# Performance work log

Measured on AMD Instinct MI355X. Metric: run time of the kernel, lower is better.

Reference implementation:

```python
import jax, jax.numpy as jnp
import numpy as np

N_HEADS = 12

def setup_inputs() -> dict:
    key = jax.random.key(0)
    ks = jax.random.split(key, 5)
    B, T, H = 8, 1024, 768
    x = jax.random.normal(ks[0], (B, T, H), dtype=jnp.float32)
    # PyTorch Linear init: U(-1/sqrt(fan_in), 1/sqrt(fan_in))
    s1 = 1.0 / np.sqrt(H)
    W_attn = jax.random.uniform(ks[1], (H, 3 * H), minval=-s1, maxval=s1, dtype=jnp.float32)
    b_attn = jax.random.uniform(ks[2], (3 * H,), minval=-s1, maxval=s1, dtype=jnp.float32)
    W_proj = jax.random.uniform(ks[3], (H, H), minval=-s1, maxval=s1, dtype=jnp.float32)
    b_proj = jax.random.uniform(ks[4], (H,), minval=-s1, maxval=s1, dtype=jnp.float32)
    return {"x": x, "W_attn": W_attn, "b_attn": b_attn, "W_proj": W_proj, "b_proj": b_proj}

def reference(x, W_attn, b_attn, W_proj, b_proj):
    B, T, H = x.shape
    nh = N_HEADS
    Hs = H // nh
    qkv = x @ W_attn + b_attn                       # [B,T,3H]
    q, k, v = jnp.split(qkv, 3, axis=-1)            # each [B,T,H]
    # -> [B, nh, T, Hs]
    q = q.reshape(B, T, nh, Hs).transpose(0, 2, 1, 3)
    k = k.reshape(B, T, nh, Hs).transpose(0, 2, 1, 3)
    v = v.reshape(B, T, nh, Hs).transpose(0, 2, 1, 3)
    scale = 1.0 / jnp.sqrt(jnp.asarray(Hs, dtype=x.dtype))
    scores = jnp.einsum("bhqd,bhkd->bhqk", q, k) * scale  # [B,nh,T,T]
    causal = jnp.tril(jnp.ones((T, T), dtype=bool))
    scores = jnp.where(causal, scores, jnp.asarray(-jnp.inf, dtype=scores.dtype))
    attn = jax.nn.softmax(scores, axis=-1)
    out = jnp.einsum("bhqk,bhkd->bhqd", attn, v)    # [B,nh,T,Hs]
    out = out.transpose(0, 2, 1, 3).reshape(B, T, H)
    return out @ W_proj + b_proj
```

## Files before the change

kernel.cpp:

```cpp
#include <hip/hip_runtime.h>
#include <math.h>


typedef __attribute__((ext_vector_type(4))) float  f32x4;
typedef __attribute__((ext_vector_type(8))) short  bf16x8;
typedef __attribute__((ext_vector_type(4))) short  bf16x4;
typedef __attribute__((ext_vector_type(4))) unsigned int u32x4;

__device__ __forceinline__ unsigned short f2bf(float f) {
    union { float f; unsigned u; } v; v.f = f;
    unsigned r = (v.u + 0x7FFFu + ((v.u >> 16) & 1u)) >> 16;
    return (unsigned short)r;
}

__device__ __forceinline__ void glds16(const unsigned short* g, unsigned short* l) {
    __builtin_amdgcn_global_load_lds((const __attribute__((address_space(1))) void*)g,
                                     (__attribute__((address_space(3))) void*)l, 16, 0, 0);
}

__global__ __launch_bounds__(256)
void cvt_f32_bf16(const float* __restrict__ in, unsigned short* __restrict__ out) {
    const int i = blockIdx.x * 256 + threadIdx.x;
    const float4 v = ((const float4*)in)[i];
    ushort4 o;
    o.x = f2bf(v.x); o.y = f2bf(v.y); o.z = f2bf(v.z); o.w = f2bf(v.w);
    ((ushort4*)out)[i] = o;
}

__global__ __launch_bounds__(256)
void transpose_w(const float* __restrict__ W, unsigned short* __restrict__ Wt,
                 int K, int N) {
    __shared__ float Ts[64][65];
    const int k0 = blockIdx.x * 64, n0 = blockIdx.y * 64;
    const int t = threadIdx.x;
    const int r = t >> 4, cg = (t & 15) * 4;
#pragma unroll
    for (int p = 0; p < 4; ++p) {
        const float4 v = *(const float4*)(&W[(size_t)(k0 + r + p * 16) * N + n0 + cg]);
        Ts[r + p * 16][cg + 0] = v.x;
        Ts[r + p * 16][cg + 1] = v.y;
        Ts[r + p * 16][cg + 2] = v.z;
        Ts[r + p * 16][cg + 3] = v.w;
    }
    __syncthreads();
#pragma unroll
    for (int p = 0; p < 4; ++p) {
        const int n = n0 + r + p * 16;
        ushort4 o;
        o.x = f2bf(Ts[cg + 0][r + p * 16]);
        o.y = f2bf(Ts[cg + 1][r + p * 16]);
        o.z = f2bf(Ts[cg + 2][r + p * 16]);
        o.w = f2bf(Ts[cg + 3][r + p * 16]);
        *(ushort4*)(&Wt[(size_t)n * K + k0 + cg]) = o;
    }
}

__global__ __launch_bounds__(256)
void gemm_bf16(const unsigned short* __restrict__ A, const unsigned short* __restrict__ Bt,
               const float* __restrict__ bias, void* __restrict__ Cout,
               int M, int N, int K, int out_bf16) {
    __shared__ unsigned short As[128 * 32];
    __shared__ unsigned short Bs[128 * 32];

    const int t = threadIdx.x;
    const int L = t & 63, w = t >> 6;
    const int l15 = L & 15, quad = L >> 4;
    const int wy = w & 1, wx = w >> 1;
    const int m0 = blockIdx.x * 128, n0 = blockIdx.y * 128;

    const int srow = t >> 2, koff = (t & 3) * 8;
    const unsigned short* ag = A + (size_t)(m0 + srow) * K + koff;
    const unsigned short* bg = Bt + (size_t)(n0 + srow) * K + koff;
    unsigned short* as0 = As + srow * 32 + koff;
    unsigned short* bs0 = Bs + srow * 32 + koff;
    const size_t gstep = (size_t)64 * K;

    f32x4 acc[4][4];
#pragma unroll
    for (int mt = 0; mt < 4; ++mt)
#pragma unroll
        for (int nt = 0; nt < 4; ++nt) acc[mt][nt] = (f32x4){0.f, 0.f, 0.f, 0.f};

    for (int k0 = 0; k0 < K; k0 += 32) {
        glds16(ag + k0,         as0);
        glds16(ag + gstep + k0, as0 + 64 * 32);
        glds16(bg + k0,         bs0);
        glds16(bg + gstep + k0, bs0 + 64 * 32);
        __syncthreads();

        bf16x8 af[4], bfr[4];
#pragma unroll
        for (int mt = 0; mt < 4; ++mt)
            af[mt] = *(const bf16x8*)(As + (wy * 64 + mt * 16 + l15) * 32 + quad * 8);
#pragma unroll
        for (int nt = 0; nt < 4; ++nt)
            bfr[nt] = *(const bf16x8*)(Bs + (wx * 64 + nt * 16 + l15) * 32 + quad * 8);
#pragma unroll
        for (int mt = 0; mt < 4; ++mt)
#pragma unroll
            for (int nt = 0; nt < 4; ++nt)
                acc[mt][nt] = __builtin_amdgcn_mfma_f32_16x16x32_bf16(af[mt], bfr[nt], acc[mt][nt], 0, 0, 0);
        __syncthreads();
    }

    float bv[4];
#pragma unroll
    for (int nt = 0; nt < 4; ++nt) bv[nt] = bias[n0 + wx * 64 + nt * 16 + l15];
#pragma unroll
    for (int mt = 0; mt < 4; ++mt) {
        const int mrow = m0 + wy * 64 + mt * 16 + quad * 4;
#pragma unroll
        for (int r = 0; r < 4; ++r) {
            const int m = mrow + r;
            if (out_bf16) {
                unsigned short* C = (unsigned short*)Cout;
#pragma unroll
                for (int nt = 0; nt < 4; ++nt)
                    C[(size_t)m * N + n0 + wx * 64 + nt * 16 + l15] = f2bf(acc[mt][nt][r] + bv[nt]);
            } else {
                float* C = (float*)Cout;
#pragma unroll
                for (int nt = 0; nt < 4; ++nt)
                    C[(size_t)m * N + n0 + wx * 64 + nt * 16 + l15] = acc[mt][nt][r] + bv[nt];
            }
        }
    }
}

__global__ __launch_bounds__(256)
void attn_mfma(const unsigned short* __restrict__ qkv, unsigned short* __restrict__ attb) {
    const int T = 1024, QKVW = 2304, NH = 12, H = 768;
    __shared__ unsigned short Ks[64 * 64];
    __shared__ unsigned short Vt[64 * 72];

    const int t = threadIdx.x;
    const int L = t & 63, w = t >> 6;
    const int l15 = L & 15, quad = L >> 4;
    const int pair = blockIdx.x & 7;
    const int bh = blockIdx.x >> 3;
    const int h = bh % NH, b = bh / NH;

    const unsigned short* base = qkv + (size_t)b * T * QKVW + h * 64;

    const int g0 = t,        r0 = g0 >> 3, lc0 = (g0 & 7) ^ (r0 & 7);
    const int g1 = 256 + t,  r1 = g1 >> 3, lc1 = (g1 & 7) ^ (r1 & 7);
    const float SM = 0.18033688f;

    for (int sub = 0; sub < 2; ++sub) {
        const int qt = sub ? pair : 15 - pair;
        const int q0 = qt * 64;

        __syncthreads();
        glds16(base + (size_t)(q0 + r0) * QKVW + lc0 * 8, Ks + g0 * 8);
        glds16(base + (size_t)(q0 + r1) * QKVW + lc1 * 8, Ks + g1 * 8);
        __syncthreads();

        bf16x8 qf[2];
        {
            const int qrow = 16 * w + l15;
            qf[0] = *(const bf16x8*)(Ks + qrow * 64 + ((quad    ) ^ (qrow & 7)) * 8);
            qf[1] = *(const bf16x8*)(Ks + qrow * 64 + ((quad + 4) ^ (qrow & 7)) * 8);
        }

        f32x4 ot[4];
#pragma unroll
        for (int dt = 0; dt < 4; ++dt) ot[dt] = (f32x4){0.f, 0.f, 0.f, 0.f};
        float mrun = -1e30f, lsum = 0.f;

        for (int j0 = 0; j0 <= q0; j0 += 64) {
            __syncthreads();
            glds16(base + (size_t)(j0 + r0) * QKVW + 768 + lc0 * 8, Ks + g0 * 8);
            glds16(base + (size_t)(j0 + r1) * QKVW + 768 + lc1 * 8, Ks + g1 * 8);
            {
                const int k4 = (t & 15) * 4, d4 = (t >> 4) * 4;
                const unsigned short* vb = base + 1536 + d4;
                const ushort4 a0 = *(const ushort4*)(vb + (size_t)(j0 + k4 + 0) * QKVW);
                const ushort4 a1 = *(const ushort4*)(vb + (size_t)(j0 + k4 + 1) * QKVW);
                const ushort4 a2 = *(const ushort4*)(vb + (size_t)(j0 + k4 + 2) * QKVW);
                const ushort4 a3 = *(const ushort4*)(vb + (size_t)(j0 + k4 + 3) * QKVW);
                ushort4 c0, c1, c2, c3;
                c0.x = a0.x; c0.y = a1.x; c0.z = a2.x; c0.w = a3.x;
                c1.x = a0.y; c1.y = a1.y; c1.z = a2.y; c1.w = a3.y;
                c2.x = a0.z; c2.y = a1.z; c2.z = a2.z; c2.w = a3.z;
                c3.x = a0.w; c3.y = a1.w; c3.z = a2.w; c3.w = a3.w;
                *(ushort4*)(Vt + (size_t)(d4 + 0) * 72 + k4) = c0;
                *(ushort4*)(Vt + (size_t)(d4 + 1) * 72 + k4) = c1;
                *(ushort4*)(Vt + (size_t)(d4 + 2) * 72 + k4) = c2;
                *(ushort4*)(Vt + (size_t)(d4 + 3) * 72 + k4) = c3;
            }
            __syncthreads();

            f32x4 st[4];
#pragma unroll
            for (int mt = 0; mt < 4; ++mt) {
                st[mt] = (f32x4){0.f, 0.f, 0.f, 0.f};
                const int krow = 16 * mt + l15;
                const bf16x8 kf0 = *(const bf16x8*)(Ks + krow * 64 + ((quad    ) ^ (krow & 7)) * 8);
                const bf16x8 kf1 = *(const bf16x8*)(Ks + krow * 64 + ((quad + 4) ^ (krow & 7)) * 8);
                st[mt] = __builtin_amdgcn_mfma_f32_16x16x32_bf16(kf0, qf[0], st[mt], 0, 0, 0);
                st[mt] = __builtin_amdgcn_mfma_f32_16x16x32_bf16(kf1, qf[1], st[mt], 0, 0, 0);
            }

            if (j0 == q0) {
                const int qin = 16 * w + l15;
#pragma unroll
                for (int mt = 0; mt < 4; ++mt)
#pragma unroll
                    for (int r = 0; r < 4; ++r)
                        if (16 * mt + 4 * quad + r > qin) st[mt][r] = -1e30f;
            }

            float nm = st[0][0];
#pragma unroll
            for (int mt = 0; mt < 4; ++mt)
#pragma unroll
                for (int r = 0; r < 4; ++r) nm = fmaxf(nm, st[mt][r]);
            nm = fmaxf(nm, __shfl_xor(nm, 16, 64));
            nm = fmaxf(nm, __shfl_xor(nm, 32, 64));
            const float mnew = fmaxf(mrun, nm);
            const float alpha = __builtin_amdgcn_exp2f((mrun - mnew) * SM);
            float ps[4][4];
            float rs = 0.f;
#pragma unroll
            for (int mt = 0; mt < 4; ++mt)
#pragma unroll
                for (int r = 0; r < 4; ++r) {
                    const float p = __builtin_amdgcn_exp2f((st[mt][r] - mnew) * SM);
                    ps[mt][r] = p; rs += p;
                }
            rs += __shfl_xor(rs, 16, 64);
            rs += __shfl_xor(rs, 32, 64);
            lsum = lsum * alpha + rs;
            mrun = mnew;
#pragma unroll
            for (int dt = 0; dt < 4; ++dt) {
                ot[dt][0] *= alpha; ot[dt][1] *= alpha; ot[dt][2] *= alpha; ot[dt][3] *= alpha;
            }

            bf16x4 pf[4];
#pragma unroll
            for (int c = 0; c < 4; ++c) {
                bf16x4 p;
                p[0] = (short)f2bf(ps[c][0]);
                p[1] = (short)f2bf(ps[c][1]);
                p[2] = (short)f2bf(ps[c][2]);
                p[3] = (short)f2bf(ps[c][3]);
                pf[c] = p;
            }

#pragma unroll
            for (int c = 0; c < 4; ++c)
#pragma unroll
                for (int dt = 0; dt < 4; ++dt) {
                    const bf16x4 vf = *(const bf16x4*)(Vt + (size_t)(16 * dt + l15) * 72 + 16 * c + 4 * quad);
                    ot[dt] = __builtin_amdgcn_mfma_f32_16x16x16bf16_1k(vf, pf[c], ot[dt], 0, 0, 0);
                }
        }

        __syncthreads();
        const float inv = 1.0f / lsum;
#pragma unroll
        for (int dt = 0; dt < 4; ++dt)
#pragma unroll
            for (int r = 0; r < 4; ++r)
                Vt[(16 * w + l15) * 72 + 16 * dt + 4 * quad + r] = f2bf(ot[dt][r] * inv);
        __syncthreads();
        {
            const int row = t & 63, hf = t >> 6;
            const u32x4 v0 = *(const u32x4*)(Vt + row * 72 + hf * 16);
            const u32x4 v1 = *(const u32x4*)(Vt + row * 72 + hf * 16 + 8);
            unsigned short* dst = attb + (size_t)(b * T + q0 + row) * H + h * 64 + hf * 16;
            *(u32x4*)dst = v0; *(u32x4*)(dst + 8) = v1;
        }
    }
}

extern "C" void kernel_launch(void* const* d_in, const int* in_sizes, int n_in,
                              void* d_out, int out_size, void* d_ws, size_t ws_size,
                              hipStream_t stream) {
    const float* x      = (const float*)d_in[0];
    const float* W_attn = (const float*)d_in[1];
    const float* b_attn = (const float*)d_in[2];
    const float* W_proj = (const float*)d_in[3];
    const float* b_proj = (const float*)d_in[4];
    float* out = (float*)d_out;

    const int Bn = 8, T = 1024, H = 768, NH = 12;
    const int M = Bn * T;
    const int N1 = 3 * H;

    unsigned short* xb   = (unsigned short*)d_ws;
    unsigned short* Wta  = xb + (size_t)M * H;
    unsigned short* Wtp  = Wta + (size_t)N1 * H;
    unsigned short* qkvb = Wtp + (size_t)H * H;
    unsigned short* attb = qkvb + (size_t)M * N1;

    dim3 blk(256);

    cvt_f32_bf16<<<dim3((M * H) / 1024), blk, 0, stream>>>(x, xb);
    transpose_w<<<dim3(H / 64, N1 / 64), blk, 0, stream>>>(W_attn, Wta, H, N1);
    transpose_w<<<dim3(H / 64, H / 64), blk, 0, stream>>>(W_proj, Wtp, H, H);

    gemm_bf16<<<dim3(M / 128, N1 / 128), blk, 0, stream>>>(xb, Wta, b_attn, qkvb, M, N1, H, 1);

    attn_mfma<<<dim3(Bn * NH * 8), blk, 0, stream>>>(qkvb, attb);

    gemm_bf16<<<dim3(M / 128, H / 128), blk, 0, stream>>>(attb, Wtp, b_proj, out, M, H, H, 0);
}
```

Measured before the change: 205.3 us.

## Double-buffer K/V tiles in attention and shrink proj GEMM M-tile

```diff
diff --git a/kernel.cpp b/kernel.cpp
--- a/kernel.cpp
+++ b/kernel.cpp
@@ -1,4 +1,5 @@
 #include <hip/hip_runtime.h>
+#include <hip/hip_bf16.h>
 #include <math.h>
 
 
@@ -11,6 +12,13 @@
     union { float f; unsigned u; } v; v.f = f;
     unsigned r = (v.u + 0x7FFFu + ((v.u >> 16) & 1u)) >> 16;
     return (unsigned short)r;
+}
+
+__device__ __forceinline__ bf16x4 pk4(float a, float b, float c, float d) {
+    union { struct { __hip_bfloat162 lo, hi; } p; bf16x4 v; } u;
+    u.p.lo = __float22bfloat162_rn(make_float2(a, b));
+    u.p.hi = __float22bfloat162_rn(make_float2(c, d));
+    return u.v;
 }
 
 __device__ __forceinline__ void glds16(const unsigned short* g, unsigned short* l) {
@@ -55,18 +63,19 @@
     }
 }
 
+template <int MT>
 __global__ __launch_bounds__(256)
 void gemm_bf16(const unsigned short* __restrict__ A, const unsigned short* __restrict__ Bt,
                const float* __restrict__ bias, void* __restrict__ Cout,
                int M, int N, int K, int out_bf16) {
-    __shared__ unsigned short As[128 * 32];
+    __shared__ unsigned short As[MT * 32 * 32];
     __shared__ unsigned short Bs[128 * 32];
 
     const int t = threadIdx.x;
     const int L = t & 63, w = t >> 6;
     const int l15 = L & 15, quad = L >> 4;
     const int wy = w & 1, wx = w >> 1;
-    const int m0 = blockIdx.x * 128, n0 = blockIdx.y * 128;
+    const int m0 = blockIdx.x * (MT * 32), n0 = blockIdx.y * 128;
 
     const int srow = t >> 2, koff = (t & 3) * 8;
     const unsigned short* ag = A + (size_t)(m0 + srow) * K + koff;
@@ -75,28 +84,28 @@
     unsigned short* bs0 = Bs + srow * 32 + koff;
     const size_t gstep = (size_t)64 * K;
 
-    f32x4 acc[4][4];
-#pragma unroll
-    for (int mt = 0; mt < 4; ++mt)
+    f32x4 acc[MT][4];
+#pragma unroll
+    for (int mt = 0; mt < MT; ++mt)
 #pragma unroll
         for (int nt = 0; nt < 4; ++nt) acc[mt][nt] = (f32x4){0.f, 0.f, 0.f, 0.f};
 
     for (int k0 = 0; k0 < K; k0 += 32) {
-        glds16(ag + k0,         as0);
-        glds16(ag + gstep + k0, as0 + 64 * 32);
-        glds16(bg + k0,         bs0);
+        glds16(ag + k0, as0);
+        if (MT == 4) glds16(ag + gstep + k0, as0 + 64 * 32);
+        glds16(bg + k0, bs0);
         glds16(bg + gstep + k0, bs0 + 64 * 32);
         __syncthreads();
 
-        bf16x8 af[4], bfr[4];
-#pragma unroll
-        for (int mt = 0; mt < 4; ++mt)
-            af[mt] = *(const bf16x8*)(As + (wy * 64 + mt * 16 + l15) * 32 + quad * 8);
+        bf16x8 af[MT], bfr[4];
+#pragma unroll
+        for (int mt = 0; mt < MT; ++mt)
+            af[mt] = *(const bf16x8*)(As + (wy * (MT * 16) + mt * 16 + l15) * 32 + quad * 8);
 #pragma unroll
         for (int nt = 0; nt < 4; ++nt)
             bfr[nt] = *(const bf16x8*)(Bs + (wx * 64 + nt * 16 + l15) * 32 + quad * 8);
 #pragma unroll
-        for (int mt = 0; mt < 4; ++mt)
+        for (int mt = 0; mt < MT; ++mt)
 #pragma unroll
             for (int nt = 0; nt < 4; ++nt)
                 acc[mt][nt] = __builtin_amdgcn_mfma_f32_16x16x32_bf16(af[mt], bfr[nt], acc[mt][nt], 0, 0, 0);
@@ -107,8 +116,8 @@
 #pragma unroll
     for (int nt = 0; nt < 4; ++nt) bv[nt] = bias[n0 + wx * 64 + nt * 16 + l15];
 #pragma unroll
-    for (int mt = 0; mt < 4; ++mt) {
-        const int mrow = m0 + wy * 64 + mt * 16 + quad * 4;
+    for (int mt = 0; mt < MT; ++mt) {
+        const int mrow = m0 + wy * (MT * 16) + mt * 16 + quad * 4;
 #pragma unroll
         for (int r = 0; r < 4; ++r) {
             const int m = mrow + r;
@@ -130,20 +139,22 @@
 __global__ __launch_bounds__(256)
 void attn_mfma(const unsigned short* __restrict__ qkv, unsigned short* __restrict__ attb) {
     const int T = 1024, QKVW = 2304, NH = 12, H = 768;
-    __shared__ unsigned short Ks[64 * 64];
-    __shared__ unsigned short Vt[64 * 72];
+    __shared__ unsigned short Qs[64 * 64];
+    __shared__ unsigned short Ks[2][64 * 64];
+    __shared__ unsigned short Vt[2][64 * 72];
 
     const int t = threadIdx.x;
     const int L = t & 63, w = t >> 6;
     const int l15 = L & 15, quad = L >> 4;
-    const int pair = blockIdx.x & 7;
-    const int bh = blockIdx.x >> 3;
+    const int bh = blockIdx.x % 96;
+    const int pair = blockIdx.x / 96;
     const int h = bh % NH, b = bh / NH;
 
     const unsigned short* base = qkv + (size_t)b * T * QKVW + h * 64;
 
-    const int g0 = t,        r0 = g0 >> 3, lc0 = (g0 & 7) ^ (r0 & 7);
-    const int g1 = 256 + t,  r1 = g1 >> 3, lc1 = (g1 & 7) ^ (r1 & 7);
+    const int g0 = t,       r0 = g0 >> 3, lc0 = (g0 & 7) ^ (r0 & 7);
+    const int g1 = 256 + t, r1 = g1 >> 3, lc1 = (g1 & 7) ^ (r1 & 7);
+    const int vk4 = (t & 15) * 4, vd4 = (t >> 4) * 4;
     const float SM = 0.18033688f;
 
     for (int sub = 0; sub < 2; ++sub) {
@@ -151,52 +162,65 @@
         const int q0 = qt * 64;
 
         __syncthreads();
-        glds16(base + (size_t)(q0 + r0) * QKVW + lc0 * 8, Ks + g0 * 8);
-        glds16(base + (size_t)(q0 + r1) * QKVW + lc1 * 8, Ks + g1 * 8);
+        glds16(base + (size_t)(q0 + r0) * QKVW + lc0 * 8, Qs + g0 * 8);
+        glds16(base + (size_t)(q0 + r1) * QKVW + lc1 * 8, Qs + g1 * 8);
+        glds16(base + (size_t)(r0) * QKVW + 768 + lc0 * 8, Ks[0] + g0 * 8);
+        glds16(base + (size_t)(r1) * QKVW + 768 + lc1 * 8, Ks[0] + g1 * 8);
+        ushort4 va0, va1, va2, va3;
+        {
+            const unsigned short* vb = base + 1536 + vd4;
+            va0 = *(const ushort4*)(vb + (size_t)(vk4 + 0) * QKVW);
+            va1 = *(const ushort4*)(vb + (size_t)(vk4 + 1) * QKVW);
+            va2 = *(const ushort4*)(vb + (size_t)(vk4 + 2) * QKVW);
+            va3 = *(const ushort4*)(vb + (size_t)(vk4 + 3) * QKVW);
+        }
         __syncthreads();
 
         bf16x8 qf[2];
         {
             const int qrow = 16 * w + l15;
-            qf[0] = *(const bf16x8*)(Ks + qrow * 64 + ((quad    ) ^ (qrow & 7)) * 8);
-            qf[1] = *(const bf16x8*)(Ks + qrow * 64 + ((quad + 4) ^ (qrow & 7)) * 8);
-        }
+            qf[0] = *(const bf16x8*)(Qs + qrow * 64 + ((quad    ) ^ (qrow & 7)) * 8);
+            qf[1] = *(const bf16x8*)(Qs + qrow * 64 + ((quad + 4) ^ (qrow & 7)) * 8);
+        }
+        {
+            ushort4 c0, c1, c2, c3;
+            c0.x = va0.x; c0.y = va1.x; c0.z = va2.x; c0.w = va3.x;
+            c1.x = va0.y; c1.y = va1.y; c1.z = va2.y; c1.w = va3.y;
+            c2.x = va0.z; c2.y = va1.z; c2.z = va2.z; c2.w = va3.z;
+            c3.x = va0.w; c3.y = va1.w; c3.z = va2.w; c3.w = va3.w;
+            *(ushort4*)(Vt[0] + (size_t)(vd4 + 0) * 72 + vk4) = c0;
+            *(ushort4*)(Vt[0] + (size_t)(vd4 + 1) * 72 + vk4) = c1;
+            *(ushort4*)(Vt[0] + (size_t)(vd4 + 2) * 72 + vk4) = c2;
+            *(ushort4*)(Vt[0] + (size_t)(vd4 + 3) * 72 + vk4) = c3;
+        }
+        __syncthreads();
 
         f32x4 ot[4];
 #pragma unroll
         for (int dt = 0; dt < 4; ++dt) ot[dt] = (f32x4){0.f, 0.f, 0.f, 0.f};
         float mrun = -1e30f, lsum = 0.f;
+        int cur = 0;
 
         for (int j0 = 0; j0 <= q0; j0 += 64) {
-            __syncthreads();
-            glds16(base + (size_t)(j0 + r0) * QKVW + 768 + lc0 * 8, Ks + g0 * 8);
-            glds16(base + (size_t)(j0 + r1) * QKVW + 768 + lc1 * 8, Ks + g1 * 8);
-            {
-                const int k4 = (t & 15) * 4, d4 = (t >> 4) * 4;
-                const unsigned short* vb = base + 1536 + d4;
-                const ushort4 a0 = *(const ushort4*)(vb + (size_t)(j0 + k4 + 0) * QKVW);
-                const ushort4 a1 = *(const ushort4*)(vb + (size_t)(j0 + k4 + 1) * QKVW);
-                const ushort4 a2 = *(const ushort4*)(vb + (size_t)(j0 + k4 + 2) * QKVW);
-                const ushort4 a3 = *(const ushort4*)(vb + (size_t)(j0 + k4 + 3) * QKVW);
-                ushort4 c0, c1, c2, c3;
-                c0.x = a0.x; c0.y = a1.x; c0.z = a2.x; c0.w = a3.x;
-                c1.x = a0.y; c1.y = a1.y; c1.z = a2.y; c1.w = a3.y;
-                c2.x = a0.z; c2.y = a1.z; c2.z = a2.z; c2.w = a3.z;
-                c3.x = a0.w; c3.y = a1.w; c3.z = a2.w; c3.w = a3.w;
-                *(ushort4*)(Vt + (size_t)(d4 + 0) * 72 + k4) = c0;
-                *(ushort4*)(Vt + (size_t)(d4 + 1) * 72 + k4) = c1;
-                *(ushort4*)(Vt + (size_t)(d4 + 2) * 72 + k4) = c2;
-                *(ushort4*)(Vt + (size_t)(d4 + 3) * 72 + k4) = c3;
-            }
-            __syncthreads();
+            const int nxt = cur ^ 1;
+            const bool more = (j0 + 64 <= q0);
+            if (more) {
+                glds16(base + (size_t)(j0 + 64 + r0) * QKVW + 768 + lc0 * 8, Ks[nxt] + g0 * 8);
+                glds16(base + (size_t)(j0 + 64 + r1) * QKVW + 768 + lc1 * 8, Ks[nxt] + g1 * 8);
+                const unsigned short* vb = base + 1536 + vd4;
+                va0 = *(const ushort4*)(vb + (size_t)(j0 + 64 + vk4 + 0) * QKVW);
+                va1 = *(const ushort4*)(vb + (size_t)(j0 + 64 + vk4 + 1) * QKVW);
+                va2 = *(const ushort4*)(vb + (size_t)(j0 + 64 + vk4 + 2) * QKVW);
+                va3 = *(const ushort4*)(vb + (size_t)(j0 + 64 + vk4 + 3) * QKVW);
+            }
 
             f32x4 st[4];
 #pragma unroll
             for (int mt = 0; mt < 4; ++mt) {
                 st[mt] = (f32x4){0.f, 0.f, 0.f, 0.f};
                 const int krow = 16 * mt + l15;
-                const bf16x8 kf0 = *(const bf16x8*)(Ks + krow * 64 + ((quad    ) ^ (krow & 7)) * 8);
-                const bf16x8 kf1 = *(const bf16x8*)(Ks + krow * 64 + ((quad + 4) ^ (krow & 7)) * 8);
+                const bf16x8 kf0 = *(const bf16x8*)(Ks[cur] + krow * 64 + ((quad    ) ^ (krow & 7)) * 8);
+                const bf16x8 kf1 = *(const bf16x8*)(Ks[cur] + krow * 64 + ((quad + 4) ^ (krow & 7)) * 8);
                 st[mt] = __builtin_amdgcn_mfma_f32_16x16x32_bf16(kf0, qf[0], st[mt], 0, 0, 0);
                 st[mt] = __builtin_amdgcn_mfma_f32_16x16x32_bf16(kf1, qf[1], st[mt], 0, 0, 0);
             }
@@ -239,36 +263,44 @@
 
             bf16x4 pf[4];
 #pragma unroll
-            for (int c = 0; c < 4; ++c) {
-                bf16x4 p;
-                p[0] = (short)f2bf(ps[c][0]);
-                p[1] = (short)f2bf(ps[c][1]);
-                p[2] = (short)f2bf(ps[c][2]);
-                p[3] = (short)f2bf(ps[c][3]);
-                pf[c] = p;
-            }
-
-#pragma unroll
             for (int c = 0; c < 4; ++c)
+                pf[c] = pk4(ps[c][0], ps[c][1], ps[c][2], ps[c][3]);
+
+            if (more) {
+                ushort4 c0, c1, c2, c3;
+                c0.x = va0.x; c0.y = va1.x; c0.z = va2.x; c0.w = va3.x;
+                c1.x = va0.y; c1.y = va1.y; c1.z = va2.y; c1.w = va3.y;
+                c2.x = va0.z; c2.y = va1.z; c2.z = va2.z; c2.w = va3.z;
+                c3.x = va0.w; c3.y = va1.w; c3.z = va2.w; c3.w = va3.w;
+                *(ushort4*)(Vt[nxt] + (size_t)(vd4 + 0) * 72 + vk4) = c0;
+                *(ushort4*)(Vt[nxt] + (size_t)(vd4 + 1) * 72 + vk4) = c1;
+                *(ushort4*)(Vt[nxt] + (size_t)(vd4 + 2) * 72 + vk4) = c2;
+                *(ushort4*)(Vt[nxt] + (size_t)(vd4 + 3) * 72 + vk4) = c3;
+            }
+
+#pragma unroll
+            for (int c = 0; c < 4; ++c)
 #pragma unroll
                 for (int dt = 0; dt < 4; ++dt) {
-                    const bf16x4 vf = *(const bf16x4*)(Vt + (size_t)(16 * dt + l15) * 72 + 16 * c + 4 * quad);
+                    const bf16x4 vf = *(const bf16x4*)(Vt[cur] + (size_t)(16 * dt + l15) * 72 + 16 * c + 4 * quad);
                     ot[dt] = __builtin_amdgcn_mfma_f32_16x16x16bf16_1k(vf, pf[c], ot[dt], 0, 0, 0);
                 }
-        }
-
-        __syncthreads();
+
+            __syncthreads();
+            cur = nxt;
+        }
+
         const float inv = 1.0f / lsum;
 #pragma unroll
         for (int dt = 0; dt < 4; ++dt)
 #pragma unroll
             for (int r = 0; r < 4; ++r)
-                Vt[(16 * w + l15) * 72 + 16 * dt + 4 * quad + r] = f2bf(ot[dt][r] * inv);
+                Vt[0][(16 * w + l15) * 72 + 16 * dt + 4 * quad + r] = f2bf(ot[dt][r] * inv);
         __syncthreads();
         {
             const int row = t & 63, hf = t >> 6;
-            const u32x4 v0 = *(const u32x4*)(Vt + row * 72 + hf * 16);
-            const u32x4 v1 = *(const u32x4*)(Vt + row * 72 + hf * 16 + 8);
+            const u32x4 v0 = *(const u32x4*)(Vt[0] + row * 72 + hf * 16);
+            const u32x4 v1 = *(const u32x4*)(Vt[0] + row * 72 + hf * 16 + 8);
             unsigned short* dst = attb + (size_t)(b * T + q0 + row) * H + h * 64 + hf * 16;
             *(u32x4*)dst = v0; *(u32x4*)(dst + 8) = v1;
         }
@@ -301,9 +333,9 @@
     transpose_w<<<dim3(H / 64, N1 / 64), blk, 0, stream>>>(W_attn, Wta, H, N1);
     transpose_w<<<dim3(H / 64, H / 64), blk, 0, stream>>>(W_proj, Wtp, H, H);
 
-    gemm_bf16<<<dim3(M / 128, N1 / 128), blk, 0, stream>>>(xb, Wta, b_attn, qkvb, M, N1, H, 1);
+    gemm_bf16<4><<<dim3(M / 128, N1 / 128), blk, 0, stream>>>(xb, Wta, b_attn, qkvb, M, N1, H, 1);
 
     attn_mfma<<<dim3(Bn * NH * 8), blk, 0, stream>>>(qkvb, attb);
 
-    gemm_bf16<<<dim3(M / 128, H / 128), blk, 0, stream>>>(attb, Wtp, b_proj, out, M, H, H, 0);
-}
+    gemm_bf16<2><<<dim3(M / 64, H / 128), blk, 0, stream>>>(attb, Wtp, b_proj, out, M, H, H, 0);
+}
```

Result: slower. 256.4 us (+24.9%).
